# Kernel optimization log

Hardware: AMD Instinct MI355X
Metric: run time of the kernel (lower is better)

Reference implementation:

```python
import math
import jax, jax.numpy as jnp
import numpy as np

B, T, C, H = 4, 2048, 1024, 16

def _rope_cos_sin(dim, max_pos):
    half = dim // 2
    pos = jnp.arange(max_pos, dtype=jnp.float32)[:, None]
    freqs = jnp.exp(jnp.arange(half, dtype=jnp.float32) * (-math.log(10000.0) / (half - 1)))[None, :]
    args = pos * freqs  # [T, half]
    return jnp.cos(args), jnp.sin(args)

def _apply_rope(x, cos, sin):
    # x: [B, H, T, D]; pairs (even, odd) along D form complex numbers
    xr = x[..., 0::2]
    xi = x[..., 1::2]
    c = cos[None, None, :, :]
    s = sin[None, None, :, :]
    out_r = xr * c - xi * s
    out_i = xr * s + xi * c
    return jnp.stack([out_r, out_i], axis=-1).reshape(x.shape)

def setup_inputs() -> dict:
    key = jax.random.key(0)
    ks = jax.random.split(key, 9)
    sc = 1.0 / math.sqrt(C)
    return {
        "x": jax.random.normal(ks[0], (B, T, C), jnp.float32),
        "Wq": jax.random.normal(ks[1], (C, C), jnp.float32) * sc,
        "bq": jax.random.normal(ks[2], (C,), jnp.float32) * 0.01,
        "Wk": jax.random.normal(ks[3], (C, C), jnp.float32) * sc,
        "bk": jax.random.normal(ks[4], (C,), jnp.float32) * 0.01,
        "Wv": jax.random.normal(ks[5], (C, C), jnp.float32) * sc,
        "bv": jax.random.normal(ks[6], (C,), jnp.float32) * 0.01,
        "Wp": jax.random.normal(ks[7], (C, C), jnp.float32) * sc,
        "bp": jax.random.normal(ks[8], (C,), jnp.float32) * 0.01,
        "n_head": H,
    }

def reference(x, Wq, bq, Wk, bk, Wv, bv, Wp, bp, n_head):
    Bx, Tx, Cx = x.shape
    D = Cx // n_head
    def heads(w, b):
        return (x @ w + b).reshape(Bx, Tx, n_head, D).transpose(0, 2, 1, 3)  # [B,H,T,D]
    q = heads(Wq, bq)
    k = heads(Wk, bk)
    v = heads(Wv, bv)
    cos, sin = _rope_cos_sin(D, Tx)
    q = _apply_rope(q, cos, sin)
    k = _apply_rope(k, cos, sin)
    att = jnp.einsum("bhtd,bhsd->bhts", q, k) * (1.0 / math.sqrt(D))
    causal = jnp.tril(jnp.ones((Tx, Tx), dtype=bool))
    att = jnp.where(causal[None, None, :, :], att, jnp.float32(-1e10))
    att = jax.nn.softmax(att, axis=-1)
    y = jnp.einsum("bhts,bhsd->bhtd", att, v)
    y = y.transpose(0, 2, 1, 3).reshape(Bx, Tx, Cx)
    return y @ Wp + bp
```

## Files before the change

### kernel.cpp

```cpp
#include <hip/hip_runtime.h>
#include <hip/hip_bf16.h>
#include <stdint.h>

namespace {

constexpr int Bx = 4, Tx = 2048, Cx = 1024, Hx = 16, Dx = 64;
constexpr int Mx = Bx * Tx;

typedef __attribute__((ext_vector_type(8))) short bf16x8;
typedef __attribute__((ext_vector_type(4))) float f32x4;
typedef __attribute__((ext_vector_type(16))) float f32x16;
typedef __attribute__((ext_vector_type(2))) unsigned int u32x2;

__device__ __forceinline__ float b2f(unsigned short u) {
  unsigned int v = ((unsigned int)u) << 16;
  return __builtin_bit_cast(float, v);
}
__device__ __forceinline__ unsigned short f2b(float f) {
  unsigned int v = __builtin_bit_cast(unsigned int, f);
  v += 0x7fffu + ((v >> 16) & 1u);
  return (unsigned short)(v >> 16);
}
__device__ __forceinline__ uint32_t pkbf(float a, float b) {
  __hip_bfloat162 h = __float22bfloat162_rn(float2{a, b});
  uint32_t r;
  __builtin_memcpy(&r, &h, 4);
  return r;
}
__device__ __forceinline__ void pl32swap(uint32_t& a, uint32_t& b) {
  u32x2 r = __builtin_amdgcn_permlane32_swap(a, b, false, false);
  a = r[0];
  b = r[1];
}

#define GLD16(g, lp) __builtin_amdgcn_global_load_lds(                     \
    (__attribute__((address_space(1))) void*)(g),                          \
    (__attribute__((address_space(3))) void*)(lp), 16, 0, 0)

__global__ void ca_cvt(const float* __restrict__ src, unsigned short* __restrict__ dst, int n4) {
  int i = blockIdx.x * blockDim.x + threadIdx.x;
  int stride = gridDim.x * blockDim.x;
  for (; i < n4; i += stride) {
    float4 f = ((const float4*)src)[i];
    ushort4 o;
    o.x = f2b(f.x); o.y = f2b(f.y); o.z = f2b(f.z); o.w = f2b(f.w);
    ((ushort4*)dst)[i] = o;
  }
}

__global__ void ca_wt4(const float* __restrict__ W0, const float* __restrict__ W1,
                       const float* __restrict__ W2, const float* __restrict__ W3,
                       unsigned short* __restrict__ Wt) {
  __shared__ float tile[32][33];
  int z = blockIdx.z;
  const float* W = z == 0 ? W0 : (z == 1 ? W1 : (z == 2 ? W2 : W3));
  unsigned short* o = Wt + (size_t)z * Cx * Cx;
  int n0 = blockIdx.x * 32, k0 = blockIdx.y * 32;
  int j = threadIdx.x & 31, i = threadIdx.x >> 5;
#pragma unroll
  for (int r = 0; r < 4; ++r)
    tile[i + 8 * r][j] = W[(size_t)(k0 + i + 8 * r) * Cx + n0 + j];
  __syncthreads();
#pragma unroll
  for (int r = 0; r < 4; ++r)
    o[(size_t)(n0 + i + 8 * r) * Cx + k0 + j] = f2b(tile[j][i + 8 * r]);
}

__global__ void ca_rtab(float* __restrict__ ct, float* __restrict__ st) {
  int idx = blockIdx.x * blockDim.x + threadIdx.x;
  int t = idx >> 5, i = idx & 31;
  float fr = expf((float)i * -0.29710775393471563f);
  float a = (float)t * fr;
  ct[idx] = cosf(a);
  st[idx] = sinf(a);
}

template <int MODE>
__global__ __launch_bounds__(256) void ca_gemm(
    const unsigned short* __restrict__ A, const unsigned short* __restrict__ Bt,
    const float* __restrict__ b0, const float* __restrict__ b1, const float* __restrict__ b2,
    const float* __restrict__ ctab, const float* __restrict__ stab,
    void* __restrict__ out, int M, int N, int K) {
  __shared__ __align__(16) unsigned short Al[2][128 * 32];
  __shared__ __align__(16) unsigned short Bl[2][128 * 32];
  int tid = threadIdx.x;
  int w = tid >> 6, l = tid & 63;
  int m0 = blockIdx.x * 128, n0 = blockIdx.y * 128;
  int wm = (w >> 1) * 64, wn = (w & 1) * 64;
  f32x4 acc[4][4] = {};

  int lr = l & 15, lk8 = (l >> 4) * 8;
  int srow = w * 32 + (l >> 2), scol = (l & 3) * 8;
  const unsigned short* ga0 = A + (size_t)(m0 + srow) * K + scol;
  const unsigned short* gb0 = Bt + (size_t)(n0 + srow) * K + scol;
  int nk = K / 32;
  auto stage = [&](int kt, int buf) {
    const unsigned short* ga = ga0 + kt * 32;
    const unsigned short* gb = gb0 + kt * 32;
    unsigned short* la = &Al[buf][w * 1024];
    unsigned short* lb = &Bl[buf][w * 1024];
    GLD16(ga, la);
    GLD16(ga + (size_t)16 * K, la + 512);
    GLD16(gb, lb);
    GLD16(gb + (size_t)16 * K, lb + 512);
  };
  stage(0, 0);
  __syncthreads();
  int cur = 0;
  for (int kt = 0; kt < nk; ++kt) {
    if (kt + 1 < nk) stage(kt + 1, cur ^ 1);
    bf16x8 af[4], bfr[4];
#pragma unroll
    for (int mi = 0; mi < 4; ++mi)
      af[mi] = *(const bf16x8*)&Al[cur][(wm + mi * 16 + lr) * 32 + lk8];
#pragma unroll
    for (int ni = 0; ni < 4; ++ni)
      bfr[ni] = *(const bf16x8*)&Bl[cur][(wn + ni * 16 + lr) * 32 + lk8];
#pragma unroll
    for (int mi = 0; mi < 4; ++mi)
#pragma unroll
      for (int ni = 0; ni < 4; ++ni)
        acc[mi][ni] = __builtin_amdgcn_mfma_f32_16x16x32_bf16(af[mi], bfr[ni], acc[mi][ni], 0, 0, 0);
    __syncthreads();
    cur ^= 1;
  }

  int lq4 = (l >> 4) * 4;
  if (MODE == 0) {
    constexpr float SC = 0.18033688011112042f;
    int which = n0 >> 10;
    int nb = n0 & 1023;
    const float* bias = which == 0 ? b0 : (which == 1 ? b1 : b2);
    unsigned short* o = (unsigned short*)out + (size_t)which * M * 1024;
    bool doRope = which < 2;
    float scl = which == 0 ? SC : 1.0f;
#pragma unroll
    for (int mi = 0; mi < 4; ++mi)
#pragma unroll
      for (int ni = 0; ni < 4; ++ni) {
        int ncol = nb + wn + ni * 16 + lr;
        float bv = bias[ncol];
        int j = (ncol & 63) >> 1;
        bool even = (ncol & 1) == 0;
#pragma unroll
        for (int rg = 0; rg < 4; ++rg) {
          int m = m0 + wm + mi * 16 + lq4 + rg;
          float val = acc[mi][ni][rg] + bv;
          if (doRope) {
            int t = m & (Tx - 1);
            float c = ctab[t * 32 + j], s = stab[t * 32 + j];
            float other = __shfl_xor(val, 1);
            float res = even ? (val * c - other * s) : (other * s + val * c);
            val = res * scl;
          }
          o[(size_t)m * 1024 + ncol] = f2b(val);
        }
      }
  } else {
    float* o = (float*)out;
#pragma unroll
    for (int mi = 0; mi < 4; ++mi)
#pragma unroll
      for (int ni = 0; ni < 4; ++ni) {
        int ncol = n0 + wn + ni * 16 + lr;
        float bv = b0[ncol];
#pragma unroll
        for (int rg = 0; rg < 4; ++rg) {
          int m = m0 + wm + mi * 16 + lq4 + rg;
          o[(size_t)m * N + ncol] = acc[mi][ni][rg] + bv;
        }
      }
  }
}

__global__ void ca_kvfl2(const unsigned short* __restrict__ k,
                         const unsigned short* __restrict__ v,
                         unsigned short* __restrict__ kfl,
                         unsigned short* __restrict__ vfl) {
  __shared__ __align__(16) unsigned short tl[64][80];
  int t0 = blockIdx.x * 64;
  int bh = blockIdx.y;
  int b = bh >> 4, h = bh & 15;
  int tid = threadIdx.x;
  const unsigned short* vb = v + (size_t)b * Tx * Cx + h * Dx;
  const unsigned short* kb = k + (size_t)b * Tx * Cx + h * Dx;

#pragma unroll
  for (int it = 0; it < 2; ++it) {
    int tt = it * 32 + (tid >> 3), d0 = (tid & 7) * 8;
    uint4 x = *(const uint4*)&vb[(size_t)(t0 + tt) * Cx + d0];
    unsigned short* u = (unsigned short*)&x;
#pragma unroll
    for (int jj = 0; jj < 8; ++jj) tl[d0 + jj][tt] = u[jj];
  }

#pragma unroll
  for (int r = 0; r < 2; ++r) {
    int slot = tid + r * 256;
    int tt = slot >> 8, c = (slot >> 6) & 3, ll = slot & 63;
    int lo = ll & 31, hi = ll >> 5;
    uint4 x = *(const uint4*)&kb[(size_t)(t0 + tt * 32 + lo) * Cx + hi * 8 + c * 16];
    unsigned short* ko = kfl + ((size_t)bh * 64 + (t0 >> 5) + tt) * 2048;
    *(uint4*)(ko + c * 512 + ll * 8) = x;
  }

  __syncthreads();
  int l = tid & 63, lo = l & 31, hi = l >> 5;
  int g = tid >> 6, tloc = g >> 1, kc = g & 1;
  int tglob = (t0 >> 5) + tloc;
  unsigned short* vo = vfl + ((size_t)bh * 64 + tglob) * 2048;
#pragma unroll
  for (int dc = 0; dc < 2; ++dc) {
    int j = dc * 2 + kc;
    uint4 x = *(const uint4*)&tl[dc * 32 + lo][tloc * 32 + hi * 8 + kc * 16];
    *(uint4*)(vo + j * 512 + l * 8) = x;
  }
}

__global__ __launch_bounds__(64) void ca_attn(
    const unsigned short* __restrict__ q, const unsigned short* __restrict__ kfl,
    const unsigned short* __restrict__ vfl, unsigned short* __restrict__ y) {
  __shared__ uint32_t els[32][33];
  int l = threadIdx.x & 63;
  int bh = blockIdx.x;
  int qt = (int)gridDim.y - 1 - (int)blockIdx.y;
  int b = bh >> 4, h16 = bh & 15;
  const unsigned short* qp = q + (size_t)b * Tx * Cx + h16 * Dx;
  const unsigned short* kb = kfl + (size_t)bh * 64 * 2048 + l * 8;
  const unsigned short* vb = vfl + (size_t)bh * 64 * 2048 + l * 8;
  int lo = l & 31, hi = l >> 5;
  constexpr float SHIFT = 20.0f;
  const uint32_t one2 = 0x3F803F80u;
  uint4 onesw{one2, one2, one2, one2};
  bf16x8 ONES = __builtin_bit_cast(bf16x8, onesw);

  int qbase = qt * 32;

  bf16x8 qf[4];
  {
    const unsigned short* qr = qp + (size_t)(qbase + lo) * Cx + hi * 8;
#pragma unroll
    for (int c = 0; c < 4; ++c) qf[c] = *(const bf16x8*)(qr + c * 16);
  }

  f32x16 acc0 = {}, acc1 = {}, sacc = {};
  int nt = qt + 1;

  uint4 rk[4], rv[4];
  auto loadK = [&](int t) {
#pragma unroll
    for (int c = 0; c < 4; ++c) rk[c] = *(const uint4*)(kb + t * 2048 + c * 512);
  };
  auto loadV = [&](int t) {
#pragma unroll
    for (int j = 0; j < 4; ++j) rv[j] = *(const uint4*)(vb + t * 2048 + j * 512);
  };
  loadK(0);
  loadV(0);

  for (int t = 0; t < nt; ++t) {
    bf16x8 kf[4], vf[4];
#pragma unroll
    for (int c = 0; c < 4; ++c) kf[c] = __builtin_bit_cast(bf16x8, rk[c]);
#pragma unroll
    for (int c = 0; c < 4; ++c) vf[c] = __builtin_bit_cast(bf16x8, rv[c]);
    if (t + 1 < nt) { loadK(t + 1); loadV(t + 1); }

    __builtin_amdgcn_s_setprio(1);
    f32x16 s = {};
    s = __builtin_amdgcn_mfma_f32_32x32x16_bf16(kf[0], qf[0], s, 0, 0, 0);
    s = __builtin_amdgcn_mfma_f32_32x32x16_bf16(kf[1], qf[1], s, 0, 0, 0);
    s = __builtin_amdgcn_mfma_f32_32x32x16_bf16(kf[2], qf[2], s, 0, 0, 0);
    s = __builtin_amdgcn_mfma_f32_32x32x16_bf16(kf[3], qf[3], s, 0, 0, 0);
    __builtin_amdgcn_s_setprio(0);

    float p[16];
    if (t == nt - 1) {
#pragma unroll
      for (int r = 0; r < 16; ++r) {
        int kvr = (r & 3) + 8 * (r >> 2) + 4 * hi;
        p[r] = (kvr > lo) ? 0.f : exp2f(s[r] - SHIFT);
      }
    } else {
#pragma unroll
      for (int r = 0; r < 16; ++r) p[r] = exp2f(s[r] - SHIFT);
    }

    uint32_t pk[8];
#pragma unroll
    for (int i = 0; i < 8; ++i) pk[i] = pkbf(p[2 * i], p[2 * i + 1]);
    pl32swap(pk[0], pk[2]);
    pl32swap(pk[1], pk[3]);
    pl32swap(pk[4], pk[6]);
    pl32swap(pk[5], pk[7]);
    uint4 xw{pk[0], pk[1], pk[2], pk[3]}, yw{pk[4], pk[5], pk[6], pk[7]};
    bf16x8 PB0 = __builtin_bit_cast(bf16x8, xw);
    bf16x8 PB1 = __builtin_bit_cast(bf16x8, yw);
    __builtin_amdgcn_s_setprio(1);
    acc0 = __builtin_amdgcn_mfma_f32_32x32x16_bf16(vf[0], PB0, acc0, 0, 0, 0);
    acc1 = __builtin_amdgcn_mfma_f32_32x32x16_bf16(vf[2], PB0, acc1, 0, 0, 0);
    sacc = __builtin_amdgcn_mfma_f32_32x32x16_bf16(ONES, PB0, sacc, 0, 0, 0);
    acc0 = __builtin_amdgcn_mfma_f32_32x32x16_bf16(vf[1], PB1, acc0, 0, 0, 0);
    acc1 = __builtin_amdgcn_mfma_f32_32x32x16_bf16(vf[3], PB1, acc1, 0, 0, 0);
    sacc = __builtin_amdgcn_mfma_f32_32x32x16_bf16(ONES, PB1, sacc, 0, 0, 0);
    __builtin_amdgcn_s_setprio(0);
  }

  float rl = __builtin_amdgcn_rcpf(sacc[0]);
#pragma unroll
  for (int dc = 0; dc < 2; ++dc) {
    f32x16 a = dc ? acc1 : acc0;
#pragma unroll
    for (int i = 0; i < 8; ++i) {
      uint32_t pkd = pkbf(a[2 * i] * rl, a[2 * i + 1] * rl);
      int d2 = (i & 1) + 4 * (i >> 1) + 2 * hi + dc * 16;
      els[lo][d2] = pkd;
    }
  }
  __syncthreads();
  unsigned short* yp = y + (size_t)b * Tx * Cx + h16 * Dx;
#pragma unroll
  for (int pp = 0; pp < 16; ++pp) {
    int qr = 2 * pp + hi;
    uint32_t val = els[qr][lo];
    *(uint32_t*)(yp + (size_t)(qbase + qr) * Cx + lo * 2) = val;
  }
}

}

extern "C" void kernel_launch(void* const* d_in, const int* in_sizes, int n_in,
                              void* d_out, int out_size, void* d_ws, size_t ws_size,
                              hipStream_t stream) {
  const float* x = (const float*)d_in[0];
  const float* Wq = (const float*)d_in[1];
  const float* bq = (const float*)d_in[2];
  const float* Wk = (const float*)d_in[3];
  const float* bk = (const float*)d_in[4];
  const float* Wv = (const float*)d_in[5];
  const float* bv = (const float*)d_in[6];
  const float* Wp = (const float*)d_in[7];
  const float* bp = (const float*)d_in[8];

  unsigned short* xb = (unsigned short*)d_ws;
  unsigned short* wt = xb + (size_t)Mx * Cx;
  float* ct = (float*)(wt + (size_t)4 * Cx * Cx);
  float* st = ct + Tx * 32;
  unsigned short* qb = (unsigned short*)(st + Tx * 32);
  unsigned short* kb = qb + (size_t)Mx * Cx;
  unsigned short* vb = kb + (size_t)Mx * Cx;
  unsigned short* vT = vb + (size_t)Mx * Cx;
  unsigned short* yb = vT + (size_t)Mx * Cx;
  unsigned short* kfl = yb + (size_t)Mx * Cx;
  unsigned short* vfl = kfl + (size_t)64 * 64 * 2048;

  ca_cvt<<<dim3(2048), dim3(256), 0, stream>>>(x, xb, Mx * Cx / 4);
  ca_wt4<<<dim3(32, 32, 4), dim3(256), 0, stream>>>(Wq, Wk, Wv, Wp, wt);
  ca_rtab<<<dim3(Tx * 32 / 256), dim3(256), 0, stream>>>(ct, st);

  ca_gemm<0><<<dim3(64, 24), dim3(256), 0, stream>>>(xb, wt, bq, bk, bv, ct, st, qb, Mx, 3072, Cx);
  ca_kvfl2<<<dim3(Tx / 64, Bx * Hx), dim3(256), 0, stream>>>(kb, vb, kfl, vfl);
  ca_attn<<<dim3(64, 64), dim3(64), 0, stream>>>(qb, kfl, vfl, yb);
  ca_gemm<1><<<dim3(64, 8), dim3(256), 0, stream>>>(yb, wt + (size_t)3 * Cx * Cx, bp,
                                                    nullptr, nullptr, nullptr, nullptr,
                                                    d_out, Mx, Cx, Cx);
}
```

Before: 215.5 us.

## Fuse K/V tile-layout scatter into QKV GEMM epilogue and drop relayout kernel

The QKV projection epilogue now writes K and V straight into the tiled kfl/vfl layouts that the attention kernel reads, so the separate ca_kvfl2 relayout kernel and the intermediate K/V buffers go away. This removes one launch and a full read and write of K and V. The GEMM grid axes are also swapped so that consecutive blocks step along N, which changes L2 reuse of the A rows. The cost is scattered 2-byte stores for K and 8-byte stores for V in place of row-contiguous stores, which may reduce write coalescing.

```diff
diff --git a/kernel.cpp b/kernel.cpp
--- a/kernel.cpp
+++ b/kernel.cpp
@@ -80,12 +80,13 @@
     const unsigned short* __restrict__ A, const unsigned short* __restrict__ Bt,
     const float* __restrict__ b0, const float* __restrict__ b1, const float* __restrict__ b2,
     const float* __restrict__ ctab, const float* __restrict__ stab,
-    void* __restrict__ out, int M, int N, int K) {
+    void* __restrict__ out, unsigned short* __restrict__ kfl, unsigned short* __restrict__ vfl,
+    int M, int N, int K) {
   __shared__ __align__(16) unsigned short Al[2][128 * 32];
   __shared__ __align__(16) unsigned short Bl[2][128 * 32];
   int tid = threadIdx.x;
   int w = tid >> 6, l = tid & 63;
-  int m0 = blockIdx.x * 128, n0 = blockIdx.y * 128;
+  int m0 = blockIdx.y * 128, n0 = blockIdx.x * 128;
   int wm = (w >> 1) * 64, wn = (w & 1) * 64;
   f32x4 acc[4][4] = {};
 
@@ -131,7 +132,7 @@
     int which = n0 >> 10;
     int nb = n0 & 1023;
     const float* bias = which == 0 ? b0 : (which == 1 ? b1 : b2);
-    unsigned short* o = (unsigned short*)out + (size_t)which * M * 1024;
+    unsigned short* o = (unsigned short*)out;
     bool doRope = which < 2;
     float scl = which == 0 ? SC : 1.0f;
 #pragma unroll
@@ -142,9 +143,12 @@
         float bv = bias[ncol];
         int j = (ncol & 63) >> 1;
         bool even = (ncol & 1) == 0;
+        int h = ncol >> 6, d = ncol & 63;
+        int m_base = m0 + wm + mi * 16 + lq4;
+        float vals[4];
 #pragma unroll
         for (int rg = 0; rg < 4; ++rg) {
-          int m = m0 + wm + mi * 16 + lq4 + rg;
+          int m = m_base + rg;
           float val = acc[mi][ni][rg] + bv;
           if (doRope) {
             int t = m & (Tx - 1);
@@ -153,7 +157,31 @@
             float res = even ? (val * c - other * s) : (other * s + val * c);
             val = res * scl;
           }
-          o[(size_t)m * 1024 + ncol] = f2b(val);
+          vals[rg] = val;
+        }
+        if (which == 0) {
+#pragma unroll
+          for (int rg = 0; rg < 4; ++rg)
+            o[(size_t)(m_base + rg) * 1024 + ncol] = f2b(vals[rg]);
+        } else if (which == 1) {
+          int bh = (m_base >> 11) * 16 + h;
+          size_t tilebase = ((size_t)bh * 64) * 2048 + (d >> 4) * 512 + (((d >> 3) & 1) * 32) * 8 + (d & 7);
+#pragma unroll
+          for (int rg = 0; rg < 4; ++rg) {
+            int t = (m_base + rg) & (Tx - 1);
+            kfl[tilebase + (size_t)(t >> 5) * 2048 + (t & 31) * 8] = f2b(vals[rg]);
+          }
+        } else {
+          int t = m_base & (Tx - 1);
+          int bh = (m_base >> 11) * 16 + h;
+          int tin = t & 31;
+          size_t base = ((size_t)bh * 64 + (t >> 5)) * 2048 +
+                        ((d >> 5) * 2 + ((tin >> 4) & 1)) * 512 +
+                        (((tin >> 3) & 1) * 32 + (d & 31)) * 8 + (tin & 7);
+          ushort4 pk4;
+          pk4.x = f2b(vals[0]); pk4.y = f2b(vals[1]);
+          pk4.z = f2b(vals[2]); pk4.w = f2b(vals[3]);
+          *(ushort4*)(vfl + base) = pk4;
         }
       }
   } else {
@@ -170,50 +198,6 @@
           o[(size_t)m * N + ncol] = acc[mi][ni][rg] + bv;
         }
       }
-  }
-}
-
-__global__ void ca_kvfl2(const unsigned short* __restrict__ k,
-                         const unsigned short* __restrict__ v,
-                         unsigned short* __restrict__ kfl,
-                         unsigned short* __restrict__ vfl) {
-  __shared__ __align__(16) unsigned short tl[64][80];
-  int t0 = blockIdx.x * 64;
-  int bh = blockIdx.y;
-  int b = bh >> 4, h = bh & 15;
-  int tid = threadIdx.x;
-  const unsigned short* vb = v + (size_t)b * Tx * Cx + h * Dx;
-  const unsigned short* kb = k + (size_t)b * Tx * Cx + h * Dx;
-
-#pragma unroll
-  for (int it = 0; it < 2; ++it) {
-    int tt = it * 32 + (tid >> 3), d0 = (tid & 7) * 8;
-    uint4 x = *(const uint4*)&vb[(size_t)(t0 + tt) * Cx + d0];
-    unsigned short* u = (unsigned short*)&x;
-#pragma unroll
-    for (int jj = 0; jj < 8; ++jj) tl[d0 + jj][tt] = u[jj];
-  }
-
-#pragma unroll
-  for (int r = 0; r < 2; ++r) {
-    int slot = tid + r * 256;
-    int tt = slot >> 8, c = (slot >> 6) & 3, ll = slot & 63;
-    int lo = ll & 31, hi = ll >> 5;
-    uint4 x = *(const uint4*)&kb[(size_t)(t0 + tt * 32 + lo) * Cx + hi * 8 + c * 16];
-    unsigned short* ko = kfl + ((size_t)bh * 64 + (t0 >> 5) + tt) * 2048;
-    *(uint4*)(ko + c * 512 + ll * 8) = x;
-  }
-
-  __syncthreads();
-  int l = tid & 63, lo = l & 31, hi = l >> 5;
-  int g = tid >> 6, tloc = g >> 1, kc = g & 1;
-  int tglob = (t0 >> 5) + tloc;
-  unsigned short* vo = vfl + ((size_t)bh * 64 + tglob) * 2048;
-#pragma unroll
-  for (int dc = 0; dc < 2; ++dc) {
-    int j = dc * 2 + kc;
-    uint4 x = *(const uint4*)&tl[dc * 32 + lo][tloc * 32 + hi * 8 + kc * 16];
-    *(uint4*)(vo + j * 512 + l * 8) = x;
   }
 }
 
@@ -347,10 +331,7 @@
   float* ct = (float*)(wt + (size_t)4 * Cx * Cx);
   float* st = ct + Tx * 32;
   unsigned short* qb = (unsigned short*)(st + Tx * 32);
-  unsigned short* kb = qb + (size_t)Mx * Cx;
-  unsigned short* vb = kb + (size_t)Mx * Cx;
-  unsigned short* vT = vb + (size_t)Mx * Cx;
-  unsigned short* yb = vT + (size_t)Mx * Cx;
+  unsigned short* yb = qb + (size_t)Mx * Cx;
   unsigned short* kfl = yb + (size_t)Mx * Cx;
   unsigned short* vfl = kfl + (size_t)64 * 64 * 2048;
 
@@ -358,10 +339,13 @@
   ca_wt4<<<dim3(32, 32, 4), dim3(256), 0, stream>>>(Wq, Wk, Wv, Wp, wt);
   ca_rtab<<<dim3(Tx * 32 / 256), dim3(256), 0, stream>>>(ct, st);
 
-  ca_gemm<0><<<dim3(64, 24), dim3(256), 0, stream>>>(xb, wt, bq, bk, bv, ct, st, qb, Mx, 3072, Cx);
-  ca_kvfl2<<<dim3(Tx / 64, Bx * Hx), dim3(256), 0, stream>>>(kb, vb, kfl, vfl);
+  ca_gemm<0><<<dim3(24, 64), dim3(256), 0, stream>>>(
+      xb, wt, bq, bk, bv,
+      ct, st, qb, kfl, vfl,
+      Mx, 3072, Cx);
   ca_attn<<<dim3(64, 64), dim3(64), 0, stream>>>(qb, kfl, vfl, yb);
-  ca_gemm<1><<<dim3(64, 8), dim3(256), 0, stream>>>(yb, wt + (size_t)3 * Cx * Cx, bp,
-                                                    nullptr, nullptr, nullptr, nullptr,
-                                                    d_out, Mx, Cx, Cx);
-}
+  ca_gemm<1><<<dim3(8, 64), dim3(256), 0, stream>>>(
+      yb, wt + (size_t)3 * Cx * Cx, bp, nullptr, nullptr,
+      nullptr, nullptr, d_out, nullptr, nullptr,
+      Mx, Cx, Cx);
+}
```

Result: no change. 216.3 us (+0.4%).
